# Performance work log

Measured on AMD Instinct MI355X. Metric: run time of the kernel, lower is better.

## Reference

```python
import jax, jax.numpy as jnp
import numpy as np

N, D, E_EDGES = 50000, 128, 800000
HEADS, REL_DIM, N_RELS, LAYERS = 4, 64, 64, 2
HD = HEADS * D  # per-head out_channels == d_model (concat=False)
LN_EPS = 1e-5
NEG_SLOPE = 0.2


def setup_inputs() -> dict:
    key = jax.random.key(0)
    ks = jax.random.split(key, 12)
    s = 0.02
    return {
        "x_flat": jax.random.normal(ks[0], (N, D), jnp.float32),
        "edge_index": jax.random.randint(ks[1], (2, E_EDGES), 0, N, jnp.int32),
        "edge_type": jax.random.randint(ks[2], (E_EDGES,), 0, N_RELS, jnp.int32),
        "rel_emb": jax.random.normal(ks[3], (N_RELS, REL_DIM), jnp.float32) * s,
        # stacked params for LAYERS GATv2Conv layers
        "Wl": jax.random.normal(ks[4], (LAYERS, D, HD), jnp.float32) * s,
        "bl": jnp.zeros((LAYERS, HD), jnp.float32),
        "Wr": jax.random.normal(ks[5], (LAYERS, D, HD), jnp.float32) * s,
        "br": jnp.zeros((LAYERS, HD), jnp.float32),
        "We": jax.random.normal(ks[6], (LAYERS, REL_DIM, HD), jnp.float32) * s,
        "att": jax.random.normal(ks[7], (LAYERS, HEADS, D), jnp.float32) * s,
        "b_out": jnp.zeros((LAYERS, D), jnp.float32),
        "ln_g": jnp.ones((LAYERS, D), jnp.float32),
        "ln_b": jnp.zeros((LAYERS, D), jnp.float32),
    }


def _gatv2_layer(h, src, dst, eattr, Wl, bl, Wr, br, We, att, b_out):
    # h: [N, D] -> per-head transforms [N, H, C]
    xl = (h @ Wl + bl).reshape(N, HEADS, D)   # source transform (messages)
    xr = (h @ Wr + br).reshape(N, HEADS, D)   # target transform
    xe = (eattr @ We).reshape(-1, HEADS, D)   # edge transform (no bias, PyG)
    # GATv2 attention: a^T leaky_relu(xl_j + xr_i + xe)
    s = jax.nn.leaky_relu(xl[src] + xr[dst] + xe, NEG_SLOPE)  # [E, H, C]
    logits = jnp.einsum('ehc,hc->eh', s, att)                  # [E, H]
    # segment softmax over destination nodes
    mx = jax.ops.segment_max(logits, dst, num_segments=N)      # [N, H]
    ex = jnp.exp(logits - mx[dst])
    den = jax.ops.segment_sum(ex, dst, num_segments=N)
    alpha = ex / den[dst]                                      # [E, H]
    msg = xl[src] * alpha[..., None]                           # [E, H, C]
    out = jax.ops.segment_sum(msg.reshape(-1, HD), dst, num_segments=N)
    out = out.reshape(N, HEADS, D).mean(axis=1) + b_out        # concat=False -> mean
    return out


def _layernorm(x, g, b):
    mu = x.mean(-1, keepdims=True)
    var = ((x - mu) ** 2).mean(-1, keepdims=True)
    return (x - mu) * jax.lax.rsqrt(var + LN_EPS) * g + b


def reference(x_flat, edge_index, edge_type, rel_emb, Wl, bl, Wr, br, We, att, b_out, ln_g, ln_b):
    src, dst = edge_index[0], edge_index[1]
    eattr = rel_emb[edge_type]  # [E, REL_DIM]
    h = x_flat
    for l in range(LAYERS):
        m = _gatv2_layer(h, src, dst, eattr, Wl[l], bl[l], Wr[l], br[l], We[l], att[l], b_out[l])
        m = jax.nn.gelu(m, approximate=False)  # dropout in eval mode
        h = _layernorm(h + m, ln_g[l], ln_b[l])
    return h
```

## Files before the change

kernel.cpp:

```cpp
#include <hip/hip_runtime.h>
#include <hip/hip_bf16.h>

#define NN 50000
#define DM 128
#define EE 800000
#define NH 4
#define HDIM 512
#define NRELS 64
#define RDIM 64
#define LAYERS 2
#define NB 196

typedef short frag8 __attribute__((ext_vector_type(8)));
typedef float f32x4 __attribute__((ext_vector_type(4)));
typedef float f32x2 __attribute__((ext_vector_type(2)));

__device__ __forceinline__ float b2f(unsigned short u) {
    unsigned v = ((unsigned)u) << 16;
    union { unsigned u; float f; } c; c.u = v; return c.f;
}
__device__ __forceinline__ float b2f_lo(unsigned u) {
    union { unsigned u; float f; } c; c.u = u << 16; return c.f;
}
__device__ __forceinline__ float b2f_hi(unsigned u) {
    union { unsigned u; float f; } c; c.u = u & 0xFFFF0000u; return c.f;
}
__device__ __forceinline__ unsigned short f2b(float f) {
    union { float f; unsigned u; } c; c.f = f;
    unsigned u = c.u;
    u += 0x7FFFu + ((u >> 16) & 1u);
    return (unsigned short)(u >> 16);
}

__global__ void count_kernel(const int* __restrict__ dst, int* __restrict__ counts) {
    int e = blockIdx.x * 256 + threadIdx.x;
    if (e < EE) atomicAdd(&counts[dst[e]], 1);
}

__global__ __launch_bounds__(256) void psum_kernel(const int* __restrict__ counts,
                                                   int* __restrict__ psums) {
    int idx = blockIdx.x * 256 + threadIdx.x;
    int x = (idx < NN) ? counts[idx] : 0;
    int lane = threadIdx.x & 63, wv = threadIdx.x >> 6;
    #pragma unroll
    for (int d = 1; d < 64; d <<= 1) x += __shfl_xor(x, d, 64);
    __shared__ int ws[4];
    if (lane == 0) ws[wv] = x;
    __syncthreads();
    if (threadIdx.x == 0) psums[blockIdx.x] = ws[0] + ws[1] + ws[2] + ws[3];
}

__global__ __launch_bounds__(256) void pscan_kernel(const int* __restrict__ psums,
                                                    int* __restrict__ offs,
                                                    int* __restrict__ row_ptr) {
    int t = threadIdx.x;
    int x = (t < NB) ? psums[t] : 0;
    int lane = t & 63, wv = t >> 6;
    int incl = x;
    #pragma unroll
    for (int d = 1; d < 64; d <<= 1) {
        int y = __shfl_up(incl, d, 64);
        if (lane >= d) incl += y;
    }
    __shared__ int ws[4];
    if (lane == 63) ws[wv] = incl;
    __syncthreads();
    int off = 0;
    for (int k = 0; k < wv; ++k) off += ws[k];
    if (t < NB) offs[t] = incl + off - x;
    if (t == 0) row_ptr[0] = 0;
}

__global__ __launch_bounds__(256) void pfin_kernel(const int* __restrict__ counts,
                                                   const int* __restrict__ offs,
                                                   int* __restrict__ row_ptr,
                                                   int* __restrict__ cursor) {
    int idx = blockIdx.x * 256 + threadIdx.x;
    int x = (idx < NN) ? counts[idx] : 0;
    int lane = threadIdx.x & 63, wv = threadIdx.x >> 6;
    int incl = x;
    #pragma unroll
    for (int d = 1; d < 64; d <<= 1) {
        int y = __shfl_up(incl, d, 64);
        if (lane >= d) incl += y;
    }
    __shared__ int ws[4];
    if (lane == 63) ws[wv] = incl;
    __syncthreads();
    int off = offs[blockIdx.x];
    for (int k = 0; k < wv; ++k) off += ws[k];
    if (idx < NN) {
        int v = off + incl;
        row_ptr[idx + 1] = v;
        cursor[idx] = v - x;
    }
}

__global__ void scatter_kernel(const int* __restrict__ dst, int* __restrict__ cursor,
                               int* __restrict__ perm) {
    int e = blockIdx.x * 256 + threadIdx.x;
    if (e < EE) {
        int p = atomicAdd(&cursor[dst[e]], 1);
        perm[p] = e;
    }
}

__global__ void wconv_all_kernel(const float* __restrict__ Wl, const float* __restrict__ Wr,
                                 unsigned short* __restrict__ Wt) {
    int idx = blockIdx.x * 256 + threadIdx.x;
    if (idx >= 4 * DM * HDIM) return;
    int m = idx >> 16;
    int r = idx & 65535;
    int c = r >> 7, k = r & 127;
    int l = m >> 1;
    const float* W = (m & 1) ? Wr : Wl;
    Wt[idx] = f2b(W[(size_t)l * DM * HDIM + k * HDIM + c]);
}

__global__ void hb_kernel(const float* __restrict__ h, unsigned short* __restrict__ hb, int n4) {
    int idx = blockIdx.x * 256 + threadIdx.x;
    if (idx >= n4) return;
    float4 v = ((const float4*)h)[idx];
    ushort4 o;
    o.x = f2b(v.x); o.y = f2b(v.y); o.z = f2b(v.z); o.w = f2b(v.w);
    ((ushort4*)hb)[idx] = o;
}

__global__ void xe_kernel(const float* __restrict__ rel_emb,
                          const float* __restrict__ We,
                          float* __restrict__ xef,
                          unsigned short* __restrict__ xeb) {
    int idx = blockIdx.x * 256 + threadIdx.x;
    if (idx >= LAYERS * NRELS * HDIM) return;
    int l  = idx / (NRELS * HDIM);
    int r  = (idx / HDIM) & (NRELS - 1);
    int hc = idx & (HDIM - 1);
    const float* Wel = We + (size_t)l * RDIM * HDIM;
    float s = 0.f;
    #pragma unroll 8
    for (int d = 0; d < RDIM; ++d) s += rel_emb[r * RDIM + d] * Wel[d * HDIM + hc];
    xef[idx] = s;
    xeb[idx] = f2b(s);
}

__global__ void be_kernel(const float* __restrict__ xef, const float* __restrict__ att,
                          float* __restrict__ be) {
    int tid = blockIdx.x * 256 + threadIdx.x;
    if (tid >= LAYERS * NRELS * NH) return;
    int l = tid >> 8;
    int r = (tid >> 2) & 63;
    int hh = tid & 3;
    const float* xp = xef + (size_t)l * NRELS * HDIM + r * HDIM + hh * DM;
    const float* ap = att + (size_t)l * HDIM + hh * DM;
    float s = 0.f;
    #pragma unroll 8
    for (int c = 0; c < DM; ++c) s += ap[c] * xp[c];
    be[tid] = 0.6f * s;
}

__global__ void edge_prep_kernel(const int* __restrict__ perm, const int* __restrict__ ei,
                                 const int* __restrict__ etype,
                                 const float* __restrict__ ab, const float* __restrict__ be_l,
                                 float* __restrict__ cle, unsigned* __restrict__ pkq) {
    int q = blockIdx.x * 256 + threadIdx.x;
    if (q >= EE) return;
    int e = perm[q];
    int s = ei[e];
    int r = etype[e];
    float4 a4 = ((const float4*)ab)[2 * s];
    float4 b4 = ((const float4*)be_l)[r];
    float4 o;
    o.x = a4.x + b4.x; o.y = a4.y + b4.y; o.z = a4.z + b4.z; o.w = a4.w + b4.w;
    ((float4*)cle)[q] = o;
    pkq[q] = ((unsigned)s << 6) | (unsigned)r;
}

__global__ __launch_bounds__(256) void gemm_xlxr_ab_kernel(
    const unsigned short* __restrict__ hb,
    const unsigned short* __restrict__ WtL,
    const unsigned short* __restrict__ WtR,
    const float* __restrict__ bl, const float* __restrict__ br,
    const float* __restrict__ att_l,
    unsigned short* __restrict__ xl, unsigned short* __restrict__ xr,
    float* __restrict__ ab) {
    int w = threadIdx.x >> 6, lane = threadIdx.x & 63;
    int m0 = blockIdx.x * 32;
    int colL = lane & 15, kg = lane >> 4;

    frag8 a[2][4];
    #pragma unroll
    for (int mt = 0; mt < 2; ++mt) {
        int row = m0 + mt * 16 + colL;
        if (row >= NN) row = NN - 1;
        const unsigned short* arow = hb + (size_t)row * DM;
        #pragma unroll
        for (int kc = 0; kc < 4; ++kc) {
            uint4 raw = *(const uint4*)(arow + kc * 32 + kg * 8);
            a[mt][kc] = __builtin_bit_cast(frag8, raw);
        }
    }

    float prow[2][2][4];
    #pragma unroll
    for (int mt = 0; mt < 2; ++mt)
        #pragma unroll
        for (int mat = 0; mat < 2; ++mat)
            #pragma unroll
            for (int r = 0; r < 4; ++r) prow[mt][mat][r] = 0.f;

    #pragma unroll
    for (int mat = 0; mat < 2; ++mat) {
        const unsigned short* Wt = mat ? WtR : WtL;
        const float* bias = mat ? br : bl;
        unsigned short* out = mat ? xr : xl;
        #pragma unroll
        for (int nt = 0; nt < 8; ++nt) {
            int col = w * 128 + nt * 16 + colL;
            f32x4 acc0 = {0.f, 0.f, 0.f, 0.f};
            f32x4 acc1 = {0.f, 0.f, 0.f, 0.f};
            #pragma unroll
            for (int kc = 0; kc < 4; ++kc) {
                uint4 raw = *(const uint4*)(Wt + (size_t)col * DM + kc * 32 + kg * 8);
                frag8 b = __builtin_bit_cast(frag8, raw);
                acc0 = __builtin_amdgcn_mfma_f32_16x16x32_bf16(a[0][kc], b, acc0, 0, 0, 0);
                acc1 = __builtin_amdgcn_mfma_f32_16x16x32_bf16(a[1][kc], b, acc1, 0, 0, 0);
            }
            float bb = bias[col];
            float ac = att_l[col];
            #pragma unroll
            for (int r = 0; r < 4; ++r) {
                float v0 = acc0[r] + bb;
                float v1 = acc1[r] + bb;
                int row0 = m0 + kg * 4 + r;
                int row1 = row0 + 16;
                if (row0 < NN) out[(size_t)row0 * HDIM + col] = f2b(v0);
                if (row1 < NN) out[(size_t)row1 * HDIM + col] = f2b(v1);
                prow[0][mat][r] = fmaf(ac, v0, prow[0][mat][r]);
                prow[1][mat][r] = fmaf(ac, v1, prow[1][mat][r]);
            }
        }
    }
    #pragma unroll
    for (int d = 1; d < 16; d <<= 1) {
        #pragma unroll
        for (int mt = 0; mt < 2; ++mt)
            #pragma unroll
            for (int mat = 0; mat < 2; ++mat)
                #pragma unroll
                for (int r = 0; r < 4; ++r)
                    prow[mt][mat][r] += __shfl_xor(prow[mt][mat][r], d, 64);
    }
    if (colL == 0) {
        #pragma unroll
        for (int mt = 0; mt < 2; ++mt) {
            int row = m0 + mt * 16 + kg * 4;
            #pragma unroll
            for (int mat = 0; mat < 2; ++mat)
                #pragma unroll
                for (int r = 0; r < 4; ++r)
                    if (row + r < NN)
                        ab[(size_t)(row + r) * 8 + mat * 4 + w] = 0.6f * prow[mt][mat][r];
        }
    }
}

__global__ __launch_bounds__(256) void node_fused_kernel(
    const int* __restrict__ row_ptr,
    const float* __restrict__ cle,
    const unsigned* __restrict__ pkq,
    const unsigned short* __restrict__ xl,
    const unsigned short* __restrict__ xr,
    const unsigned short* __restrict__ xeb_l,
    const float* __restrict__ ab,
    const float* __restrict__ att_l,
    const float* __restrict__ h_in,
    const float* __restrict__ b_out, const float* __restrict__ ln_g,
    const float* __restrict__ ln_b,
    float* __restrict__ h_out,
    unsigned short* __restrict__ hb_out) {
    int w = threadIdx.x >> 6, l = threadIdx.x & 63;
    int i = blockIdx.x * 4 + w;
    int hh = l >> 4;
    __shared__ float cl[4][64][4];

    int beg = row_ptr[i], end = row_ptr[i + 1];
    int c0 = (l & 15) * 8;

    uint4 xrv = *(const uint4*)(xr + (size_t)i * HDIM + l * 8);
    f32x2 xrp0 = f32x2{b2f_lo(xrv.x), b2f_hi(xrv.x)};
    f32x2 xrp1 = f32x2{b2f_lo(xrv.y), b2f_hi(xrv.y)};
    f32x2 xrp2 = f32x2{b2f_lo(xrv.z), b2f_hi(xrv.z)};
    f32x2 xrp3 = f32x2{b2f_lo(xrv.w), b2f_hi(xrv.w)};
    float4 at0 = ((const float4*)(att_l + l * 8))[0];
    float4 at1 = ((const float4*)(att_l + l * 8))[1];
    float atv[8] = {at0.x * 0.4f, at0.y * 0.4f, at0.z * 0.4f, at0.w * 0.4f,
                    at1.x * 0.4f, at1.y * 0.4f, at1.z * 0.4f, at1.w * 0.4f};
    float4 bxv = ((const float4*)ab)[2 * i + 1];
    float4 hv0 = *(const float4*)(h_in + (size_t)i * DM + c0);
    float4 hv1 = *(const float4*)(h_in + (size_t)i * DM + c0 + 4);

    const char* xl_b = (const char*)xl;
    const char* xe_b = (const char*)xeb_l;
    uint l16 = (uint)l << 4;

    float ss = 0.f;
    f32x2 acc0 = f32x2{0.f, 0.f}, acc1 = f32x2{0.f, 0.f};
    f32x2 acc2 = f32x2{0.f, 0.f}, acc3 = f32x2{0.f, 0.f};

    for (int cb = beg; cb < end; cb += 64) {
        int mc = min(64, end - cb);
        unsigned pkr = 0;
        if (l < mc) {
            float4 c4 = ((const float4*)cle)[cb + l];
            pkr = pkq[cb + l];
            cl[w][l][0] = c4.x + bxv.x;
            cl[w][l][1] = c4.y + bxv.y;
            cl[w][l][2] = c4.z + bxv.z;
            cl[w][l][3] = c4.w + bxv.w;
        }
        unsigned pk0 = __shfl(pkr, 0, 64);
        uint4 vvP = *(const uint4*)(xl_b + ((pk0 >> 6) << 10) + l16);
        uint4 eeP = *(const uint4*)(xe_b + ((pk0 & 63u) << 10) + l16);
        float cjP = cl[w][0][hh];
        for (int j = 1; j <= mc; ++j) {
            uint4 vv = vvP; uint4 ee = eeP; float cj = cjP;
            if (j < mc) {
                unsigned pkj = __shfl(pkr, j, 64);
                vvP = *(const uint4*)(xl_b + ((pkj >> 6) << 10) + l16);
                eeP = *(const uint4*)(xe_b + ((pkj & 63u) << 10) + l16);
                cjP = cl[w][j][hh];
            }
            f32x2 xp0 = f32x2{b2f_lo(vv.x), b2f_hi(vv.x)};
            f32x2 xp1 = f32x2{b2f_lo(vv.y), b2f_hi(vv.y)};
            f32x2 xp2 = f32x2{b2f_lo(vv.z), b2f_hi(vv.z)};
            f32x2 xp3 = f32x2{b2f_lo(vv.w), b2f_hi(vv.w)};
            f32x2 z0 = (xp0 + xrp0) + f32x2{b2f_lo(ee.x), b2f_hi(ee.x)};
            f32x2 z1 = (xp1 + xrp1) + f32x2{b2f_lo(ee.y), b2f_hi(ee.y)};
            f32x2 z2 = (xp2 + xrp2) + f32x2{b2f_lo(ee.z), b2f_hi(ee.z)};
            f32x2 z3 = (xp3 + xrp3) + f32x2{b2f_lo(ee.w), b2f_hi(ee.w)};
            float partial = fmaf(atv[0], fabsf(z0[0]),
                            fmaf(atv[1], fabsf(z0[1]),
                            fmaf(atv[2], fabsf(z1[0]),
                            fmaf(atv[3], fabsf(z1[1]),
                            fmaf(atv[4], fabsf(z2[0]),
                            fmaf(atv[5], fabsf(z2[1]),
                            fmaf(atv[6], fabsf(z3[0]), atv[7] * fabsf(z3[1]))))))));
            #pragma unroll
            for (int d = 1; d < 16; d <<= 1) partial += __shfl_xor(partial, d, 64);
            float we = __expf(partial + cj);
            ss += we;
            f32x2 wv = f32x2{we, we};
            acc0 += wv * xp0;
            acc1 += wv * xp1;
            acc2 += wv * xp2;
            acc3 += wv * xp3;
        }
    }

    float invs = (ss > 0.f) ? 1.f / ss : 0.f;
    float sv[8] = {acc0[0] * invs, acc0[1] * invs, acc1[0] * invs, acc1[1] * invs,
                   acc2[0] * invs, acc2[1] * invs, acc3[0] * invs, acc3[1] * invs};
    #pragma unroll
    for (int d = 16; d < 64; d <<= 1)
        #pragma unroll
        for (int k = 0; k < 8; ++k) sv[k] += __shfl_xor(sv[k], d, 64);

    float4 bo0 = *(const float4*)(b_out + c0);
    float4 bo1 = *(const float4*)(b_out + c0 + 4);
    float bov[8] = {bo0.x, bo0.y, bo0.z, bo0.w, bo1.x, bo1.y, bo1.z, bo1.w};
    float hvv[8] = {hv0.x, hv0.y, hv0.z, hv0.w, hv1.x, hv1.y, hv1.z, hv1.w};
    float yv[8];
    float la = 0.f, lb = 0.f;
    #pragma unroll
    for (int k = 0; k < 8; ++k) {
        float o = sv[k] * 0.25f + bov[k];
        float ge = 0.5f * o * (1.f + erff(o * 0.70710678118654752f));
        float y = hvv[k] + ge;
        yv[k] = y; la += y; lb += y * y;
    }
    #pragma unroll
    for (int d = 1; d < 16; d <<= 1) {
        la += __shfl_xor(la, d, 64);
        lb += __shfl_xor(lb, d, 64);
    }
    float mean = la * (1.f / 128.f);
    float var = lb * (1.f / 128.f) - mean * mean;
    float rs = rsqrtf(var + 1e-5f);

    if (l < 16) {
        float4 g0 = *(const float4*)(ln_g + c0);
        float4 g1 = *(const float4*)(ln_g + c0 + 4);
        float4 q0 = *(const float4*)(ln_b + c0);
        float4 q1 = *(const float4*)(ln_b + c0 + 4);
        float gv[8] = {g0.x, g0.y, g0.z, g0.w, g1.x, g1.y, g1.z, g1.w};
        float qv[8] = {q0.x, q0.y, q0.z, q0.w, q1.x, q1.y, q1.z, q1.w};
        float ov[8];
        #pragma unroll
        for (int k = 0; k < 8; ++k)
            ov[k] = (yv[k] - mean) * rs * gv[k] + qv[k];
        float* hop = h_out + (size_t)i * DM + c0;
        *(float4*)hop = make_float4(ov[0], ov[1], ov[2], ov[3]);
        *(float4*)(hop + 4) = make_float4(ov[4], ov[5], ov[6], ov[7]);
        uint4 ob;
        ob.x = (unsigned)f2b(ov[0]) | ((unsigned)f2b(ov[1]) << 16);
        ob.y = (unsigned)f2b(ov[2]) | ((unsigned)f2b(ov[3]) << 16);
        ob.z = (unsigned)f2b(ov[4]) | ((unsigned)f2b(ov[5]) << 16);
        ob.w = (unsigned)f2b(ov[6]) | ((unsigned)f2b(ov[7]) << 16);
        *(uint4*)(hb_out + (size_t)i * DM + c0) = ob;
    }
}

extern "C" void kernel_launch(void* const* d_in, const int* in_sizes, int n_in,
                              void* d_out, int out_size, void* d_ws, size_t ws_size,
                              hipStream_t stream) {
    const float* x_flat   = (const float*)d_in[0];
    const int*   edge_idx = (const int*)d_in[1];
    const int*   edge_ty  = (const int*)d_in[2];
    const float* rel_emb  = (const float*)d_in[3];
    const float* Wl       = (const float*)d_in[4];
    const float* bl       = (const float*)d_in[5];
    const float* Wr       = (const float*)d_in[6];
    const float* br       = (const float*)d_in[7];
    const float* We       = (const float*)d_in[8];
    const float* att      = (const float*)d_in[9];
    const float* b_out    = (const float*)d_in[10];
    const float* ln_g     = (const float*)d_in[11];
    const float* ln_b     = (const float*)d_in[12];

    char* p = (char*)d_ws;
    auto carve = [&](size_t bytes) {
        void* r = (void*)p;
        p += (bytes + 255) & ~(size_t)255;
        return r;
    };
    unsigned short* xl     = (unsigned short*)carve((size_t)NN * HDIM * 2);
    unsigned short* xr     = (unsigned short*)carve((size_t)NN * HDIM * 2);
    float*          h1     = (float*)carve((size_t)NN * DM * 4);
    unsigned short* hb     = (unsigned short*)carve((size_t)NN * DM * 2);
    unsigned short* Wt     = (unsigned short*)carve((size_t)4 * DM * HDIM * 2);
    float*          xef    = (float*)carve((size_t)LAYERS * NRELS * HDIM * 4);
    unsigned short* xeb    = (unsigned short*)carve((size_t)LAYERS * NRELS * HDIM * 2);
    float*          ab     = (float*)carve((size_t)NN * 8 * 4);
    float*          be     = (float*)carve((size_t)LAYERS * NRELS * NH * 4);
    int*            row_ptr= (int*)carve((size_t)(NN + 1) * 4);
    int*            counts = (int*)carve((size_t)NN * 4);
    int*            cursor = (int*)carve((size_t)NN * 4);
    int*            perm   = (int*)carve((size_t)EE * 4);
    int*            psums  = (int*)carve((size_t)NB * 4);
    int*            offs   = (int*)carve((size_t)NB * 4);
    float*          cle    = (float*)carve((size_t)EE * 4 * 4);
    unsigned*       pkq    = (unsigned*)carve((size_t)EE * 4);

    const int* dst = edge_idx + EE;

    hipMemsetAsync(counts, 0, (size_t)NN * 4, stream);
    count_kernel<<<(EE + 255) / 256, 256, 0, stream>>>(dst, counts);
    psum_kernel<<<NB, 256, 0, stream>>>(counts, psums);
    pscan_kernel<<<1, 256, 0, stream>>>(psums, offs, row_ptr);
    pfin_kernel<<<NB, 256, 0, stream>>>(counts, offs, row_ptr, cursor);
    scatter_kernel<<<(EE + 255) / 256, 256, 0, stream>>>(dst, cursor, perm);

    wconv_all_kernel<<<(4 * DM * HDIM + 255) / 256, 256, 0, stream>>>(Wl, Wr, Wt);
    xe_kernel<<<(LAYERS * NRELS * HDIM + 255) / 256, 256, 0, stream>>>(rel_emb, We, xef, xeb);
    be_kernel<<<(LAYERS * NRELS * NH + 255) / 256, 256, 0, stream>>>(xef, att, be);
    hb_kernel<<<(NN * DM / 4 + 255) / 256, 256, 0, stream>>>(x_flat, hb, NN * DM / 4);

    const float* h_cur = x_flat;
    for (int l = 0; l < LAYERS; ++l) {
        float* h_next = (l == LAYERS - 1) ? (float*)d_out : h1;
        gemm_xlxr_ab_kernel<<<(NN + 31) / 32, 256, 0, stream>>>(
            hb,
            Wt + (size_t)(l * 2 + 0) * DM * HDIM,
            Wt + (size_t)(l * 2 + 1) * DM * HDIM,
            bl + (size_t)l * HDIM, br + (size_t)l * HDIM,
            att + (size_t)l * HDIM,
            xl, xr, ab);
        edge_prep_kernel<<<(EE + 255) / 256, 256, 0, stream>>>(
            perm, edge_idx, edge_ty, ab, be + (size_t)l * NRELS * NH, cle, pkq);
        node_fused_kernel<<<NN / 4, 256, 0, stream>>>(
            row_ptr, cle, pkq, xl, xr,
            xeb + (size_t)l * NRELS * HDIM,
            ab,
            att + (size_t)l * HDIM,
            h_cur,
            b_out + (size_t)l * DM, ln_g + (size_t)l * DM, ln_b + (size_t)l * DM,
            h_next, hb);
        h_cur = h_next;
    }
}
```

Baseline: 627.0 us.

## Fuse edge prep into node kernel, merge setup kernels, use DPP reductions

Drops the per-layer edge_prep kernel and its cle buffer. The node kernel now gathers ab[src] and be[rel] on the fly from the packed (src,rel) word, which the scatter kernel writes directly in CSR order instead of a perm array. The setup kernels (bf16 conversion of h, weight transpose, xe, be, counts zeroing) are merged into one multi-role launch, and be is computed algebraically through att·We. Wave reductions switch from shfl_xor to DPP row ops. The gathered loads move into the latency-sensitive node loop in exchange for fewer launches and less memory traffic.

Result: faster. 558.3 us (-11.0%).

```diff
diff --git a/kernel.cpp b/kernel.cpp
--- a/kernel.cpp
+++ b/kernel.cpp
@@ -11,6 +11,12 @@
 #define LAYERS 2
 #define NB 196
 
+#define PM_HB 6250
+#define PM_WC 1024
+#define PM_XE 256
+#define PM_CZ 196
+#define PM_TOT (PM_HB + PM_WC + PM_XE + PM_CZ + 1)
+
 typedef short frag8 __attribute__((ext_vector_type(8)));
 typedef float f32x4 __attribute__((ext_vector_type(4)));
 typedef float f32x2 __attribute__((ext_vector_type(2)));
@@ -30,6 +36,13 @@
     unsigned u = c.u;
     u += 0x7FFFu + ((u >> 16) & 1u);
     return (unsigned short)(u >> 16);
+}
+
+template<int CTRL>
+__device__ __forceinline__ float dpp_add(float x) {
+    int yi = __builtin_amdgcn_update_dpp(0, __builtin_bit_cast(int, x),
+                                         CTRL, 0xF, 0xF, true);
+    return x + __builtin_bit_cast(float, yi);
 }
 
 __global__ void count_kernel(const int* __restrict__ dst, int* __restrict__ counts) {
@@ -96,83 +109,87 @@
     }
 }
 
-__global__ void scatter_kernel(const int* __restrict__ dst, int* __restrict__ cursor,
-                               int* __restrict__ perm) {
+__global__ void scatter_pk_kernel(const int* __restrict__ ei, const int* __restrict__ etype,
+                                  int* __restrict__ cursor, unsigned* __restrict__ pkq) {
     int e = blockIdx.x * 256 + threadIdx.x;
     if (e < EE) {
-        int p = atomicAdd(&cursor[dst[e]], 1);
-        perm[p] = e;
-    }
-}
-
-__global__ void wconv_all_kernel(const float* __restrict__ Wl, const float* __restrict__ Wr,
-                                 unsigned short* __restrict__ Wt) {
-    int idx = blockIdx.x * 256 + threadIdx.x;
-    if (idx >= 4 * DM * HDIM) return;
-    int m = idx >> 16;
-    int r = idx & 65535;
-    int c = r >> 7, k = r & 127;
-    int l = m >> 1;
-    const float* W = (m & 1) ? Wr : Wl;
-    Wt[idx] = f2b(W[(size_t)l * DM * HDIM + k * HDIM + c]);
-}
-
-__global__ void hb_kernel(const float* __restrict__ h, unsigned short* __restrict__ hb, int n4) {
-    int idx = blockIdx.x * 256 + threadIdx.x;
-    if (idx >= n4) return;
-    float4 v = ((const float4*)h)[idx];
-    ushort4 o;
-    o.x = f2b(v.x); o.y = f2b(v.y); o.z = f2b(v.z); o.w = f2b(v.w);
-    ((ushort4*)hb)[idx] = o;
-}
-
-__global__ void xe_kernel(const float* __restrict__ rel_emb,
-                          const float* __restrict__ We,
-                          float* __restrict__ xef,
-                          unsigned short* __restrict__ xeb) {
-    int idx = blockIdx.x * 256 + threadIdx.x;
-    if (idx >= LAYERS * NRELS * HDIM) return;
-    int l  = idx / (NRELS * HDIM);
-    int r  = (idx / HDIM) & (NRELS - 1);
-    int hc = idx & (HDIM - 1);
-    const float* Wel = We + (size_t)l * RDIM * HDIM;
-    float s = 0.f;
-    #pragma unroll 8
-    for (int d = 0; d < RDIM; ++d) s += rel_emb[r * RDIM + d] * Wel[d * HDIM + hc];
-    xef[idx] = s;
-    xeb[idx] = f2b(s);
-}
-
-__global__ void be_kernel(const float* __restrict__ xef, const float* __restrict__ att,
-                          float* __restrict__ be) {
-    int tid = blockIdx.x * 256 + threadIdx.x;
-    if (tid >= LAYERS * NRELS * NH) return;
-    int l = tid >> 8;
-    int r = (tid >> 2) & 63;
-    int hh = tid & 3;
-    const float* xp = xef + (size_t)l * NRELS * HDIM + r * HDIM + hh * DM;
-    const float* ap = att + (size_t)l * HDIM + hh * DM;
-    float s = 0.f;
-    #pragma unroll 8
-    for (int c = 0; c < DM; ++c) s += ap[c] * xp[c];
-    be[tid] = 0.6f * s;
-}
-
-__global__ void edge_prep_kernel(const int* __restrict__ perm, const int* __restrict__ ei,
-                                 const int* __restrict__ etype,
-                                 const float* __restrict__ ab, const float* __restrict__ be_l,
-                                 float* __restrict__ cle, unsigned* __restrict__ pkq) {
-    int q = blockIdx.x * 256 + threadIdx.x;
-    if (q >= EE) return;
-    int e = perm[q];
-    int s = ei[e];
-    int r = etype[e];
-    float4 a4 = ((const float4*)ab)[2 * s];
-    float4 b4 = ((const float4*)be_l)[r];
-    float4 o;
-    o.x = a4.x + b4.x; o.y = a4.y + b4.y; o.z = a4.z + b4.z; o.w = a4.w + b4.w;
-    ((float4*)cle)[q] = o;
-    pkq[q] = ((unsigned)s << 6) | (unsigned)r;
+        int d = ei[EE + e];
+        int p = atomicAdd(&cursor[d], 1);
+        pkq[p] = ((unsigned)ei[e] << 6) | (unsigned)etype[e];
+    }
+}
+
+__global__ __launch_bounds__(256) void prep_misc_kernel(
+    const float* __restrict__ x_flat,
+    const float* __restrict__ Wl, const float* __restrict__ Wr,
+    const float* __restrict__ rel_emb, const float* __restrict__ We,
+    const float* __restrict__ att,
+    unsigned short* __restrict__ hb, unsigned short* __restrict__ Wt,
+    unsigned short* __restrict__ xeb, float* __restrict__ be,
+    int* __restrict__ counts) {
+    int b = blockIdx.x, t = threadIdx.x;
+    if (b < PM_HB) {
+        int idx = b * 256 + t;
+        float4 v = ((const float4*)x_flat)[idx];
+        ushort4 o;
+        o.x = f2b(v.x); o.y = f2b(v.y); o.z = f2b(v.z); o.w = f2b(v.w);
+        ((ushort4*)hb)[idx] = o;
+        return;
+    }
+    b -= PM_HB;
+    if (b < PM_WC) {
+        int idx = b * 256 + t;
+        int m = idx >> 16;
+        int r = idx & 65535;
+        int c = r >> 7, k = r & 127;
+        int l = m >> 1;
+        const float* W = (m & 1) ? Wr : Wl;
+        Wt[idx] = f2b(W[(size_t)l * DM * HDIM + k * HDIM + c]);
+        return;
+    }
+    b -= PM_WC;
+    if (b < PM_XE) {
+        int idx = b * 256 + t;
+        int l  = idx / (NRELS * HDIM);
+        int r  = (idx / HDIM) & (NRELS - 1);
+        int hc = idx & (HDIM - 1);
+        const float* Wel = We + (size_t)l * RDIM * HDIM;
+        float s = 0.f;
+        #pragma unroll 8
+        for (int d = 0; d < RDIM; ++d) s += rel_emb[r * RDIM + d] * Wel[d * HDIM + hc];
+        xeb[idx] = f2b(s);
+        return;
+    }
+    b -= PM_XE;
+    if (b < PM_CZ) {
+        int idx = b * 256 + t;
+        if (idx < NN) counts[idx] = 0;
+        return;
+    }
+    __shared__ float aw_s[LAYERS * NH * RDIM];
+    #pragma unroll
+    for (int k = 0; k < 2; ++k) {
+        int idx = t * 2 + k;
+        int l = idx >> 8, h = (idx >> 6) & 3, d = idx & 63;
+        const float* ap = att + (size_t)l * HDIM + h * DM;
+        const float* wp = We + (size_t)l * RDIM * HDIM + (size_t)d * HDIM + h * DM;
+        float s = 0.f;
+        #pragma unroll 8
+        for (int c = 0; c < DM; ++c) s += ap[c] * wp[c];
+        aw_s[idx] = s;
+    }
+    __syncthreads();
+    #pragma unroll
+    for (int k = 0; k < 2; ++k) {
+        int idx = t * 2 + k;
+        int l = idx >> 8, r = (idx >> 2) & 63, h = idx & 3;
+        const float* rp = rel_emb + r * RDIM;
+        const float* ap = aw_s + l * 256 + h * 64;
+        float s = 0.f;
+        #pragma unroll 8
+        for (int d = 0; d < RDIM; ++d) s += rp[d] * ap[d];
+        be[idx] = 0.6f * s;
+    }
 }
 
 __global__ __launch_bounds__(256) void gemm_xlxr_ab_kernel(
@@ -266,12 +283,12 @@
 
 __global__ __launch_bounds__(256) void node_fused_kernel(
     const int* __restrict__ row_ptr,
-    const float* __restrict__ cle,
     const unsigned* __restrict__ pkq,
     const unsigned short* __restrict__ xl,
     const unsigned short* __restrict__ xr,
     const unsigned short* __restrict__ xeb_l,
     const float* __restrict__ ab,
+    const float* __restrict__ be_l,
     const float* __restrict__ att_l,
     const float* __restrict__ h_in,
     const float* __restrict__ b_out, const float* __restrict__ ln_g,
@@ -282,6 +299,7 @@
     int i = blockIdx.x * 4 + w;
     int hh = l >> 4;
     __shared__ float cl[4][64][4];
+    __shared__ unsigned pk_s[4][64];
 
     int beg = row_ptr[i], end = row_ptr[i + 1];
     int c0 = (l & 15) * 8;
@@ -309,23 +327,25 @@
 
     for (int cb = beg; cb < end; cb += 64) {
         int mc = min(64, end - cb);
-        unsigned pkr = 0;
         if (l < mc) {
-            float4 c4 = ((const float4*)cle)[cb + l];
-            pkr = pkq[cb + l];
-            cl[w][l][0] = c4.x + bxv.x;
-            cl[w][l][1] = c4.y + bxv.y;
-            cl[w][l][2] = c4.z + bxv.z;
-            cl[w][l][3] = c4.w + bxv.w;
+            unsigned pk = pkq[cb + l];
+            pk_s[w][l] = pk;
+            int s = pk >> 6, r = pk & 63;
+            float4 a4 = ((const float4*)ab)[2 * s];
+            float4 b4 = ((const float4*)be_l)[r];
+            cl[w][l][0] = a4.x + b4.x + bxv.x;
+            cl[w][l][1] = a4.y + b4.y + bxv.y;
+            cl[w][l][2] = a4.z + b4.z + bxv.z;
+            cl[w][l][3] = a4.w + b4.w + bxv.w;
         }
-        unsigned pk0 = __shfl(pkr, 0, 64);
+        unsigned pk0 = pk_s[w][0];
         uint4 vvP = *(const uint4*)(xl_b + ((pk0 >> 6) << 10) + l16);
         uint4 eeP = *(const uint4*)(xe_b + ((pk0 & 63u) << 10) + l16);
         float cjP = cl[w][0][hh];
         for (int j = 1; j <= mc; ++j) {
             uint4 vv = vvP; uint4 ee = eeP; float cj = cjP;
             if (j < mc) {
-                unsigned pkj = __shfl(pkr, j, 64);
+                unsigned pkj = pk_s[w][j];
                 vvP = *(const uint4*)(xl_b + ((pkj >> 6) << 10) + l16);
                 eeP = *(const uint4*)(xe_b + ((pkj & 63u) << 10) + l16);
                 cjP = cl[w][j][hh];
@@ -345,8 +365,10 @@
                             fmaf(atv[4], fabsf(z2[0]),
                             fmaf(atv[5], fabsf(z2[1]),
                             fmaf(atv[6], fabsf(z3[0]), atv[7] * fabsf(z3[1]))))))));
-            #pragma unroll
-            for (int d = 1; d < 16; d <<= 1) partial += __shfl_xor(partial, d, 64);
+            partial = dpp_add<0xB1>(partial);
+            partial = dpp_add<0x4E>(partial);
+            partial = dpp_add<0x124>(partial);
+            partial = dpp_add<0x128>(partial);
             float we = __expf(partial + cj);
             ss += we;
             f32x2 wv = f32x2{we, we};
@@ -378,11 +400,10 @@
         float y = hvv[k] + ge;
         yv[k] = y; la += y; lb += y * y;
     }
-    #pragma unroll
-    for (int d = 1; d < 16; d <<= 1) {
-        la += __shfl_xor(la, d, 64);
-        lb += __shfl_xor(lb, d, 64);
-    }
+    la = dpp_add<0xB1>(la); la = dpp_add<0x4E>(la);
+    la = dpp_add<0x124>(la); la = dpp_add<0x128>(la);
+    lb = dpp_add<0xB1>(lb); lb = dpp_add<0x4E>(lb);
+    lb = dpp_add<0x124>(lb); lb = dpp_add<0x128>(lb);
     float mean = la * (1.f / 128.f);
     float var = lb * (1.f / 128.f) - mean * mean;
     float rs = rsqrtf(var + 1e-5f);
@@ -438,32 +459,26 @@
     float*          h1     = (float*)carve((size_t)NN * DM * 4);
     unsigned short* hb     = (unsigned short*)carve((size_t)NN * DM * 2);
     unsigned short* Wt     = (unsigned short*)carve((size_t)4 * DM * HDIM * 2);
-    float*          xef    = (float*)carve((size_t)LAYERS * NRELS * HDIM * 4);
     unsigned short* xeb    = (unsigned short*)carve((size_t)LAYERS * NRELS * HDIM * 2);
     float*          ab     = (float*)carve((size_t)NN * 8 * 4);
     float*          be     = (float*)carve((size_t)LAYERS * NRELS * NH * 4);
     int*            row_ptr= (int*)carve((size_t)(NN + 1) * 4);
     int*            counts = (int*)carve((size_t)NN * 4);
     int*            cursor = (int*)carve((size_t)NN * 4);
-    int*            perm   = (int*)carve((size_t)EE * 4);
     int*            psums  = (int*)carve((size_t)NB * 4);
     int*            offs   = (int*)carve((size_t)NB * 4);
-    float*          cle    = (float*)carve((size_t)EE * 4 * 4);
     unsigned*       pkq    = (unsigned*)carve((size_t)EE * 4);
 
     const int* dst = edge_idx + EE;
 
-    hipMemsetAsync(counts, 0, (size_t)NN * 4, stream);
+    prep_misc_kernel<<<PM_TOT, 256, 0, stream>>>(
+        x_flat, Wl, Wr, rel_emb, We, att, hb, Wt, xeb, be, counts);
+
     count_kernel<<<(EE + 255) / 256, 256, 0, stream>>>(dst, counts);
     psum_kernel<<<NB, 256, 0, stream>>>(counts, psums);
     pscan_kernel<<<1, 256, 0, stream>>>(psums, offs, row_ptr);
     pfin_kernel<<<NB, 256, 0, stream>>>(counts, offs, row_ptr, cursor);
-    scatter_kernel<<<(EE + 255) / 256, 256, 0, stream>>>(dst, cursor, perm);
-
-    wconv_all_kernel<<<(4 * DM * HDIM + 255) / 256, 256, 0, stream>>>(Wl, Wr, Wt);
-    xe_kernel<<<(LAYERS * NRELS * HDIM + 255) / 256, 256, 0, stream>>>(rel_emb, We, xef, xeb);
-    be_kernel<<<(LAYERS * NRELS * NH + 255) / 256, 256, 0, stream>>>(xef, att, be);
-    hb_kernel<<<(NN * DM / 4 + 255) / 256, 256, 0, stream>>>(x_flat, hb, NN * DM / 4);
+    scatter_pk_kernel<<<(EE + 255) / 256, 256, 0, stream>>>(edge_idx, edge_ty, cursor, pkq);
 
     const float* h_cur = x_flat;
     for (int l = 0; l < LAYERS; ++l) {
@@ -475,12 +490,10 @@
             bl + (size_t)l * HDIM, br + (size_t)l * HDIM,
             att + (size_t)l * HDIM,
             xl, xr, ab);
-        edge_prep_kernel<<<(EE + 255) / 256, 256, 0, stream>>>(
-            perm, edge_idx, edge_ty, ab, be + (size_t)l * NRELS * NH, cle, pkq);
         node_fused_kernel<<<NN / 4, 256, 0, stream>>>(
-            row_ptr, cle, pkq, xl, xr,
+            row_ptr, pkq, xl, xr,
             xeb + (size_t)l * NRELS * HDIM,
-            ab,
+            ab, be + (size_t)l * NRELS * NH,
             att + (size_t)l * HDIM,
             h_cur,
             b_out + (size_t)l * DM, ln_g + (size_t)l * DM, ln_b + (size_t)l * DM,
```
